# Kernel tuning notes

Measured on AMD Instinct MI355X. Metric: run time of the kernel, lower is better.

Reference implementation:

```python
import jax, jax.numpy as jnp
import numpy as np

N_QUBITS = 12
N_LAYERS = 3
HID = 16
IN_DIM = 6
BATCH = 4096
C64 = jnp.complex64


def _ry(t):
    c = jnp.cos(t / 2).astype(C64)
    s = jnp.sin(t / 2).astype(C64)
    return jnp.stack([jnp.stack([c, -s], -1), jnp.stack([s, c], -1)], -2)


def _rx(t):
    c = jnp.cos(t / 2).astype(C64)
    s = jnp.sin(t / 2).astype(C64)
    js = 1j * s
    return jnp.stack([jnp.stack([c, -js], -1), jnp.stack([-js, c], -1)], -2)


def _rz(t):
    e = jnp.exp(-1j * t.astype(C64) / 2)
    z = jnp.zeros_like(e)
    return jnp.stack([jnp.stack([e, z], -1), jnp.stack([z, jnp.conj(e)], -1)], -2)


def _apply_1q(state, U, wire):
    # state: (B,) + (2,)*n ; U: (2,2) shared or (B,2,2) per-sample
    s = jnp.moveaxis(state, wire + 1, 1)
    if U.ndim == 2:
        s = jnp.einsum('ij,bj...->bi...', U, s)
    else:
        s = jnp.einsum('bij,bj...->bi...', U, s)
    return jnp.moveaxis(s, 1, wire + 1)


def _cnot(state, c, t):
    ax_c = c + 1
    s0 = jnp.take(state, 0, axis=ax_c)
    s1 = jnp.take(state, 1, axis=ax_c)
    t_ax = t + 1 if t < c else t  # target axis after removing control axis
    s1 = jnp.flip(s1, axis=t_ax)  # X on target when control=1
    return jnp.stack([s0, s1], axis=ax_c)


def _quantum(angles, qparams):
    # angles: (B, n_qubits) angle-encoding RY rotations; qparams: (L, n, 3)
    B = angles.shape[0]
    n = N_QUBITS
    state = jnp.zeros((B,) + (2,) * n, C64).at[(slice(None),) + (0,) * n].set(1.0)
    for i in range(n):
        state = _apply_1q(state, _ry(angles[:, i]), i)
    for l in range(N_LAYERS):
        for i in range(n):
            # RX then RY then RZ on wire i -> fused 2x2
            U = _rz(qparams[l, i, 2]) @ _ry(qparams[l, i, 1]) @ _rx(qparams[l, i, 0])
            state = _apply_1q(state, U, i)
        for i in range(n - 1):
            state = _cnot(state, i, i + 1)
        if n > 2:
            state = _cnot(state, n - 1, 0)
    p = state.real ** 2 + state.imag ** 2  # (B,) + (2,)*n
    evs = []
    for i in range(n):
        axes = tuple(a for a in range(1, n + 1) if a != i + 1)
        pi = p.sum(axes)  # (B, 2)
        evs.append(pi[:, 0] - pi[:, 1])
    return jnp.stack(evs, axis=1)  # (B, n) PauliZ expvals


def setup_inputs() -> dict:
    key = jax.random.key(0)
    ks = jax.random.split(key, 14)
    w = lambda k, shape: jax.random.normal(k, shape, jnp.float32) * 0.1
    return {
        'x': jax.random.normal(ks[0], (BATCH, IN_DIM), jnp.float32),
        'W1': w(ks[1], (HID, IN_DIM)), 'b1': w(ks[2], (HID,)),
        'W2': w(ks[3], (HID, HID)), 'b2': w(ks[4], (HID,)),
        'W3': w(ks[5], (N_QUBITS, HID)), 'b3': w(ks[6], (N_QUBITS,)),
        'qparams': w(ks[7], (N_LAYERS, N_QUBITS, 3)),
        'P1': w(ks[8], (HID, N_QUBITS)), 'c1': w(ks[9], (HID,)),
        'P2': w(ks[10], (8, HID)), 'c2': w(ks[11], (8,)),
        'P3': w(ks[12], (1, 8)), 'c3': w(ks[13], (1,)),
    }


def reference(x, W1, b1, W2, b2, W3, b3, qparams, P1, c1, P2, c2, P3, c3):
    # classical preprocessor (dropout = identity at inference)
    h = jax.nn.relu(x @ W1.T + b1)
    h = jax.nn.relu(h @ W2.T + b2)
    angles = h @ W3.T + b3  # (B, n_qubits)
    q = _quantum(angles, qparams)  # (B, n_qubits)
    # classical postprocessor
    o = jax.nn.relu(q @ P1.T + c1)
    o = jax.nn.relu(o @ P2.T + c2)
    o = jax.nn.sigmoid(o @ P3.T + c3)
    return o.squeeze(-1)  # (B,)
```

## Files before the change

### kernel.cpp

```cpp
#include <hip/hip_runtime.h>
#include <stdint.h>

#define NQ   12
#define DIM  4096
#define TPB  256

typedef float   v2f   __attribute__((ext_vector_type(2)));
typedef float   v4f   __attribute__((ext_vector_type(4)));
typedef float   f32x4 __attribute__((ext_vector_type(4)));
typedef _Float16 v2h  __attribute__((ext_vector_type(2)));
typedef _Float16 f16x8 __attribute__((ext_vector_type(8)));
typedef uint32_t u32x4 __attribute__((ext_vector_type(4)));

struct PassP {
  uint16_t v[4];
  uint16_t m[4];
  uint16_t td[4];
  uint8_t  np[8];
  uint8_t  wire[4];
  uint8_t  layer;
  uint8_t  pad[3];
};
struct KP {
  PassP    pass[6];
  uint16_t ro_mask[12];
  uint8_t  ro_bin[12];
};

constexpr int chbit(uint32_t x) { int b = -1; for (int i = 0; i < 32; ++i) if ((x >> i) & 1u) b = i; return b; }

constexpr void bmm(uint32_t* C, const uint32_t* A, const uint32_t* B) {
  for (int i = 0; i < NQ; ++i) {
    uint32_t r = 0;
    for (int j = 0; j < NQ; ++j) if ((A[i] >> j) & 1u) r ^= B[j];
    C[i] = r;
  }
}
constexpr void binv(const uint32_t* M, uint32_t* Inv) {
  uint32_t A[NQ] = {}, I[NQ] = {};
  for (int i = 0; i < NQ; ++i) { A[i] = M[i]; I[i] = 1u << i; }
  for (int c = 0; c < NQ; ++c) {
    int piv = -1;
    for (int r = c; r < NQ; ++r) if ((A[r] >> c) & 1u) { piv = r; break; }
    if (piv < 0) continue;
    uint32_t ta = A[c]; A[c] = A[piv]; A[piv] = ta;
    uint32_t ti = I[c]; I[c] = I[piv]; I[piv] = ti;
    for (int r = 0; r < NQ; ++r)
      if (r != c && ((A[r] >> c) & 1u)) { A[r] ^= A[c]; I[r] ^= I[c]; }
  }
  for (int i = 0; i < NQ; ++i) Inv[i] = I[i];
}

constexpr int rank5(const uint32_t* cols, int n) {
  uint32_t rows[5] = {}; int rnk = 0;
  for (int q = 0; q < n; ++q) {
    uint32_t x = cols[q] & 31u;
    for (int bit = 4; bit >= 0; --bit) {
      if (!((x >> bit) & 1u)) continue;
      if (rows[bit]) { x ^= rows[bit]; }
      else { rows[bit] = x; ++rnk; break; }
    }
  }
  return rnk;
}

constexpr KP make_kp() {
  KP kp{};
  uint32_t A[NQ] = {}; A[0] = 0xFFEu;
  for (int i = 1; i < NQ; ++i) A[i] = (1u << (i + 1)) - 1u;
  uint32_t A2[NQ] = {}, A3[NQ] = {}, Ai[NQ] = {}, A2i[NQ] = {};
  bmm(A2, A, A); bmm(A3, A2, A);
  binv(A, Ai); binv(A2, A2i);

  uint32_t v5_0 = 0, v5_3 = 0, td5_1 = 0, td5_2 = 0;

  for (int p = 0; p < 6; ++p) {
    const int L = (p < 3) ? 1 : 2;
    const int wb = (p % 3) * 4;
    const uint32_t* M  = (L == 1) ? A  : A2;
    const uint32_t* Mi = (L == 1) ? Ai : A2i;
    uint32_t v0[4] = {}, m0[4] = {};
    for (int i = 0; i < 4; ++i) {
      int w = wb + i; uint32_t col = 0;
      for (int r = 0; r < NQ; ++r) col |= ((Mi[r] >> w) & 1u) << r;
      v0[i] = col; m0[i] = M[w];
    }
    uint32_t Bc[NQ] = {};
    for (int b = 0; b < NQ; ++b) {
      uint32_t col = 1u << b;
      for (int i = 0; i < 4; ++i) if ((m0[i] >> b) & 1u) col ^= v0[i];
      Bc[b] = col;
    }
    uint32_t redv[4] = {}; int pbit[4] = {}; uint32_t pivmask = 0;
    for (int i = 0; i < 4; ++i) {
      redv[i] = v0[i];
      for (int k2 = 0; k2 < i; ++k2) if ((redv[i] >> pbit[k2]) & 1u) redv[i] ^= redv[k2];
      pbit[i] = chbit(redv[i]); pivmask |= 1u << pbit[i];
    }
    uint8_t np0[8] = {}; int nc = 0;
    for (int b = 0; b < NQ; ++b) if (!((pivmask >> b) & 1u)) np0[nc++] = (uint8_t)b;

    int bestScore = -1;
    int bsel[4] = {0,1,2,3}; int bT0 = 4, bT1 = 5; int bperm[4] = {0,1,2,3};
    int cand = 0;
    for (int a = 0; a < 8; ++a) for (int b = a + 1; b < 8; ++b)
    for (int c = b + 1; c < 8; ++c) for (int d = c + 1; d < 8; ++d) {
      uint32_t jc[4] = {Bc[np0[a]], Bc[np0[b]], Bc[np0[c]], Bc[np0[d]]};
      int rJ = rank5(jc, 4);
      if (rJ < 4 && bestScore >= 0) continue;
      if (rJ == 4) { if (cand >= 4) continue; ++cand; }
      int rem[4] = {}; int rc2 = 0;
      for (int q = 0; q < 8; ++q) if (q != a && q != b && q != c && q != d) rem[rc2++] = q;
      const int tmax = (p == 5) ? 4 : 1;
      for (int t0 = 0; t0 < tmax; ++t0) for (int t1 = 0; t1 < tmax; ++t1) {
        if (p != 5) { if (t0 != 0 || t1 != 0) continue; }
        else if (t1 == t0) continue;
        const int rt0 = (p == 5) ? t0 : 0, rt1 = (p == 5) ? t1 : 1;
        for (int pa = 0; pa < 4; ++pa) for (int pb2 = 0; pb2 < 4; ++pb2) {
          if (pb2 == pa) continue;
          for (int pc = 0; pc < 4; ++pc) {
            if (pc == pa || pc == pb2) continue;
            const int pd = 6 - pa - pb2 - pc;
            uint32_t rd[6] = {jc[0], jc[1], jc[2], jc[3], v0[pc], v0[pd]};
            int rR = rank5(rd, 6);
            uint32_t wr[6] = {jc[0], jc[1], jc[2], jc[3], v0[pb2], v0[pc]};
            int rW = rank5(wr, 6);
            int rRO = 0;
            if (p == 5) {
              uint32_t roc[6] = {jc[0], jc[1], jc[2], jc[3], Bc[np0[rem[rt0]]], Bc[np0[rem[rt1]]]};
              rRO = rank5(roc, 6);
            }
            int score = rJ * 1000 + (rR == 5 ? 100 : 0) + (rW == 5 ? 10 : 0)
                      + (p == 5 ? (rRO == 5 ? 1 : 0) : 0);
            if (score > bestScore) {
              bestScore = score;
              bsel[0] = a; bsel[1] = b; bsel[2] = c; bsel[3] = d;
              bT0 = rem[rt0]; bT1 = rem[rt1];
              bperm[0] = pa; bperm[1] = pb2; bperm[2] = pc; bperm[3] = pd;
            }
          }
        }
      }
    }
    uint8_t npn[8] = {};
    npn[0] = np0[bsel[0]]; npn[1] = np0[bsel[1]];
    npn[2] = np0[bsel[2]]; npn[3] = np0[bsel[3]];
    npn[4] = np0[bT0]; npn[5] = np0[bT1];
    int cn = 6;
    for (int q = 0; q < 8; ++q) {
      bool used = (q == bsel[0] || q == bsel[1] || q == bsel[2] || q == bsel[3] ||
                   q == bT0 || q == bT1);
      if (!used) npn[cn++] = np0[q];
    }
    for (int q = 0; q < 8; ++q) kp.pass[p].np[q] = npn[q];
    for (int i = 0; i < 4; ++i) {
      kp.pass[p].v[i] = (uint16_t)v0[bperm[i]];
      kp.pass[p].m[i] = (uint16_t)m0[bperm[i]];
      kp.pass[p].wire[i] = (uint8_t)(wb + bperm[i]);
    }
    kp.pass[p].td[0] = 0;
    kp.pass[p].td[1] = (uint16_t)Bc[npn[4]];
    kp.pass[p].td[2] = (uint16_t)Bc[npn[5]];
    kp.pass[p].td[3] = (uint16_t)(Bc[npn[4]] ^ Bc[npn[5]]);
    kp.pass[p].layer = (uint8_t)L;
    if (p == 5) {
      v5_0 = v0[bperm[0]]; v5_3 = v0[bperm[3]];
      td5_1 = Bc[npn[4]]; td5_2 = Bc[npn[5]];
    }
  }
  for (int i = 0; i < NQ; ++i) kp.ro_mask[i] = (uint16_t)A3[i];
  for (int i = 0; i < NQ; ++i) {
    uint32_t b = 0;
    b |= (uint32_t)(__builtin_popcount(A3[i] & v5_0) & 1) << 0;
    b |= (uint32_t)(__builtin_popcount(A3[i] & v5_3) & 1) << 1;
    b |= (uint32_t)(__builtin_popcount(A3[i] & td5_1) & 1) << 2;
    b |= (uint32_t)(__builtin_popcount(A3[i] & td5_2) & 1) << 3;
    kp.ro_bin[i] = (uint8_t)b;
  }
  return kp;
}

constexpr KP kpc = make_kp();

__device__ __forceinline__ v2f cmulf(v2f a, v2f b) {
  return (v2f){a.x * b.x - a.y * b.y, a.x * b.y + a.y * b.x};
}
__device__ __forceinline__ uint32_t f2h2(float a, float b) {
  return __builtin_bit_cast(uint32_t, __builtin_amdgcn_cvt_pkrtz(a, b));
}
__device__ __forceinline__ uint32_t pk_rtn(float a, float b) {
  v2h h = {(_Float16)a, (_Float16)b};
  return __builtin_bit_cast(uint32_t, h);
}

__device__ __forceinline__ void build_u(const float* __restrict__ qp, int l, int w, float U[8]) {
  float p0 = qp[(l * 12 + w) * 3 + 0];
  float p1 = qp[(l * 12 + w) * 3 + 1];
  float p2 = qp[(l * 12 + w) * 3 + 2];
  float cx, sx, cy, sy, cz, sz;
  sincosf(0.5f * p0, &sx, &cx);
  sincosf(0.5f * p1, &sy, &cy);
  sincosf(0.5f * p2, &sz, &cz);
  float M00x =  cy * cx, M00y =  sy * sx;
  float M01x = -sy * cx, M01y = -cy * sx;
  float M10x =  sy * cx, M10y = -cy * sx;
  float M11x =  cy * cx, M11y = -sy * sx;
  U[0] = cz * M00x + sz * M00y; U[1] = cz * M00y - sz * M00x;
  U[2] = cz * M01x + sz * M01y; U[3] = cz * M01y - sz * M01x;
  U[4] = cz * M10x - sz * M10y; U[5] = cz * M10y + sz * M10x;
  U[6] = cz * M11x - sz * M11y; U[7] = cz * M11y + sz * M11x;
}

__device__ __forceinline__ int am_col(int c, int i) {
  return ((((c >> 2) ^ ((i >> 1) & 3)) << 2) | (c & 3));
}

template<int P, bool LAST>
__device__ __forceinline__ void do_pass(uint32_t* st, f16x8 a0, f16x8 a1,
                                        int lane, int wv, float* ev) {
  constexpr PassP pp = kpc.pass[P];
  const int t6 = (lane & 15) | (wv << 6);
  int rep = 0;
  #pragma unroll
  for (int k = 0; k < 8; ++k) rep |= ((t6 >> k) & 1) << pp.np[k];
  int base = rep;
  #pragma unroll
  for (int i = 0; i < 4; ++i)
    if (__popc(pp.m[i] & rep) & 1) base ^= pp.v[i];
  const int g = lane >> 4;
  const int cgr = ((g & 1) ? pp.v[2] : 0) ^ ((g & 2) ? pp.v[3] : 0);
  const int cgw = ((g & 1) ? pp.v[1] : 0) ^ ((g & 2) ? pp.v[2] : 0);
  float pr[16];
  const f32x4 z = {0.f, 0.f, 0.f, 0.f};
  #pragma unroll
  for (int T = 0; T < 4; ++T) {
    const int bT = base ^ pp.td[T];
    const int ra = bT ^ cgr;
    u32x4 braw = { st[ra], st[ra ^ pp.v[0]], st[ra ^ pp.v[1]],
                   st[ra ^ (pp.v[0] ^ pp.v[1])] };
    f16x8 bf = __builtin_bit_cast(f16x8, braw);
    f32x4 c0 = __builtin_amdgcn_mfma_f32_16x16x32_f16(a0, bf, z, 0, 0, 0);
    f32x4 c1 = __builtin_amdgcn_mfma_f32_16x16x32_f16(a1, bf, z, 0, 0, 0);
    if constexpr (!LAST) {
      const int wa = bT ^ cgw;
      st[wa]                      = f2h2(c0.x, c0.y);
      st[wa ^ pp.v[0]]            = f2h2(c0.z, c0.w);
      st[wa ^ pp.v[3]]            = f2h2(c1.x, c1.y);
      st[wa ^ (pp.v[3] ^ pp.v[0])] = f2h2(c1.z, c1.w);
    } else {
      const int nb = ((T & 1) << 2) | ((T >> 1) << 3);
      pr[nb]     = c0.x * c0.x + c0.y * c0.y;
      pr[nb | 1] = c0.z * c0.z + c0.w * c0.w;
      pr[nb | 2] = c1.x * c1.x + c1.y * c1.y;
      pr[nb | 3] = c1.z * c1.z + c1.w * c1.w;
    }
  }
  if constexpr (LAST) {
    #pragma unroll
    for (int gs = 1; gs < 16; gs <<= 1) {
      #pragma unroll
      for (int j = 0; j < 16; ++j) {
        if (j & gs) continue;
        float u = pr[j], w2 = pr[j | gs];
        pr[j] = u + w2; pr[j | gs] = u - w2;
      }
    }
    const int baseL = base ^ cgw;
    #pragma unroll
    for (int i = 0; i < NQ; ++i) {
      float h = pr[kpc.ro_bin[i]];
      int s = (__popc(kpc.ro_mask[i] & baseL) & 1) << 31;
      ev[i] = __int_as_float(__float_as_int(h) ^ s);
    }
  }
}

__global__ __launch_bounds__(TPB, 5) void hqc_kernel(
    const float* __restrict__ x,  const float* __restrict__ W1, const float* __restrict__ b1,
    const float* __restrict__ W2, const float* __restrict__ b2,
    const float* __restrict__ W3, const float* __restrict__ b3,
    const float* __restrict__ qp, const float* __restrict__ P1, const float* __restrict__ c1,
    const float* __restrict__ P2, const float* __restrict__ c2,
    const float* __restrict__ P3, const float* __restrict__ c3,
    float* __restrict__ out)
{
  __shared__ uint32_t st[DIM];
  __shared__ __align__(16) uint32_t Am[6][32][16];
  __shared__ v2f  gg[2][12][4];
  __shared__ v4f  gpk0[12][2];
  __shared__ float red[4][NQ];

  const int s    = blockIdx.x;
  const int t    = threadIdx.x;
  const int lane = t & 63;
  const int wv   = t >> 6;
  const int g    = lane >> 4;

  if (wv == 0) {
    if (lane < 16) {
      float a = b1[lane];
      #pragma unroll
      for (int k = 0; k < 6; ++k) a = fmaf(W1[lane * 6 + k], x[s * 6 + k], a);
      float h1 = fmaxf(a, 0.f);
      float a2 = b2[lane];
      #pragma unroll
      for (int k = 0; k < 16; ++k) a2 = fmaf(W2[lane * 16 + k], __shfl(h1, k, 64), a2);
      float h2 = fmaxf(a2, 0.f);
      const int lw = (lane < NQ) ? lane : 0;
      float a3 = b3[lw];
      #pragma unroll
      for (int k = 0; k < 16; ++k) a3 = fmaf(W3[lw * 16 + k], __shfl(h2, k, 64), a3);
      if (lane < NQ) {
        float U[8]; build_u(qp, 0, lane, U);
        float ca, sa; sincosf(0.5f * a3, &sa, &ca);
        float c0x = U[0] * ca + U[2] * sa, c0y = U[1] * ca + U[3] * sa;
        float c1x = U[4] * ca + U[6] * sa, c1y = U[5] * ca + U[7] * sa;
        gpk0[lane][0] = (v4f){c0x, c0x, -c0y, c0y};
        gpk0[lane][1] = (v4f){c1x, c1x, -c1y, c1y};
      }
    }
  } else if (wv <= 2) {
    if (lane < NQ) {
      float U[8]; build_u(qp, wv, lane, U);
      gg[wv - 1][lane][0] = (v2f){U[0], U[1]};
      gg[wv - 1][lane][1] = (v2f){U[2], U[3]};
      gg[wv - 1][lane][2] = (v2f){U[4], U[5]};
      gg[wv - 1][lane][3] = (v2f){U[6], U[7]};
    }
  }
  __syncthreads();

  {
    const int r_ = t >> 4, c_ = t & 15;
    #pragma unroll
    for (int p = 0; p < 6; ++p) {
      v2f e = (v2f){1.f, 0.f};
      #pragma unroll
      for (int i = 0; i < 4; ++i) {
        v2f u = gg[kpc.pass[p].layer - 1][kpc.pass[p].wire[i]]
                  [(((r_ >> i) & 1) << 1) | ((c_ >> i) & 1)];
        e = cmulf(e, u);
      }
      const int i0 = 2 * r_, i1 = 2 * r_ + 1;
      Am[p][i0][am_col(c_, i0)] = pk_rtn(e.x, -e.y);
      Am[p][i1][am_col(c_, i1)] = pk_rtn(e.y, e.x);
    }
  }

  {
    v2f acc = (v2f){1.f, 0.f};
    #pragma unroll
    for (int i = 0; i < 8; ++i) {
      v4f gk = gpk0[i][(t >> i) & 1];
      acc = gk.xy * acc + gk.zw * acc.yx;
    }
    v2f l16[16];
    l16[0] = acc;
    #pragma unroll
    for (int i = 0; i < 4; ++i) {
      v4f g0 = gpk0[8 + i][0], g1 = gpk0[8 + i][1];
      #pragma unroll
      for (int j = 0; j < (1 << i); ++j) {
        v2f a = l16[j];
        l16[j | (1 << i)] = g1.xy * a + g1.zw * a.yx;
        l16[j]            = g0.xy * a + g0.zw * a.yx;
      }
    }
    #pragma unroll
    for (int j = 0; j < 16; ++j) st[t | (j << 8)] = f2h2(l16[j].x, l16[j].y);
  }
  __syncthreads();

  f16x8 af[6][2];
  #pragma unroll
  for (int p = 0; p < 6; ++p) {
    #pragma unroll
    for (int Rb = 0; Rb < 2; ++Rb) {
      const int i = Rb * 16 + (lane & 15);
      const int q = g ^ ((i >> 1) & 3);
      const u32x4* src = reinterpret_cast<const u32x4*>(&Am[p][i][q * 4]);
      af[p][Rb] = __builtin_bit_cast(f16x8, *src);
    }
  }

  float ev[NQ];
  do_pass<0, false>(st, af[0][0], af[0][1], lane, wv, ev); __syncthreads();
  do_pass<1, false>(st, af[1][0], af[1][1], lane, wv, ev); __syncthreads();
  do_pass<2, false>(st, af[2][0], af[2][1], lane, wv, ev); __syncthreads();
  do_pass<3, false>(st, af[3][0], af[3][1], lane, wv, ev); __syncthreads();
  do_pass<4, false>(st, af[4][0], af[4][1], lane, wv, ev); __syncthreads();
  do_pass<5, true >(st, af[5][0], af[5][1], lane, wv, ev);

  #pragma unroll
  for (int off = 32; off >= 1; off >>= 1) {
    #pragma unroll
    for (int i = 0; i < NQ; ++i) ev[i] += __shfl_xor(ev[i], off, 64);
  }
  if (lane == 0) {
    #pragma unroll
    for (int i = 0; i < NQ; ++i) red[wv][i] = ev[i];
  }
  __syncthreads();

  if (wv == 0 && lane < 16) {
    float q = (lane < NQ)
      ? (red[0][lane] + red[1][lane] + red[2][lane] + red[3][lane])
      : 0.f;
    float a = c1[lane];
    #pragma unroll
    for (int j = 0; j < NQ; ++j) a = fmaf(P1[lane * NQ + j], __shfl(q, j, 64), a);
    float o1 = fmaxf(a, 0.f);
    float a2 = c2[lane & 7];
    #pragma unroll
    for (int j = 0; j < 16; ++j) a2 = fmaf(P2[(lane & 7) * 16 + j], __shfl(o1, j, 64), a2);
    float o2 = fmaxf(a2, 0.f);
    float a3 = c3[0];
    #pragma unroll
    for (int j = 0; j < 8; ++j) a3 = fmaf(P3[j], __shfl(o2, j, 64), a3);
    if (lane == 0) out[s] = 1.f / (1.f + expf(-a3));
  }
}

extern "C" void kernel_launch(void* const* d_in, const int* in_sizes, int n_in,
                              void* d_out, int out_size, void* d_ws, size_t ws_size,
                              hipStream_t stream) {
  (void)in_sizes; (void)n_in; (void)d_ws; (void)ws_size;
  hqc_kernel<<<out_size, TPB, 0, stream>>>(
      (const float*)d_in[0],  (const float*)d_in[1],  (const float*)d_in[2],
      (const float*)d_in[3],  (const float*)d_in[4],  (const float*)d_in[5],
      (const float*)d_in[6],  (const float*)d_in[7],  (const float*)d_in[8],
      (const float*)d_in[9],  (const float*)d_in[10], (const float*)d_in[11],
      (const float*)d_in[12], (const float*)d_in[13],
      (float*)d_out);
}
```

Before: 57.67 us.

## Double-buffer per-pass gate matrices and build them just in time

Instead of building all six 4-wire gate matrices up front and keeping them in registers, the kernel now keeps a two-slot LDS buffer and builds the next pass's matrix inside the current pass. The fragments are loaded from LDS at the start of each pass. This shrinks LDS and register use so launch bounds can rise from 5 to 7 blocks per CU. The compile-time basis search is also replaced by a penalty-based cost that no longer picks readout target columns, which may change the bank-conflict pattern of pass memory accesses.

```diff
diff --git a/kernel.cpp b/kernel.cpp
--- a/kernel.cpp
+++ b/kernel.cpp
@@ -21,10 +21,9 @@
   uint8_t  layer;
   uint8_t  pad[3];
 };
-struct KP {
-  PassP    pass[6];
-  uint16_t ro_mask[12];
-  uint8_t  ro_bin[12];
+struct ROC {
+  uint16_t mask[12];
+  uint8_t  bin[12];
 };
 
 constexpr int chbit(uint32_t x) { int b = -1; for (int i = 0; i < 32; ++i) if ((x >> i) & 1u) b = i; return b; }
@@ -63,124 +62,126 @@
   }
   return rnk;
 }
-
-constexpr KP make_kp() {
-  KP kp{};
+constexpr int penalty(int r) {
+  return r >= 5 ? 0 : r == 4 ? 58 : r == 3 ? 194 : r == 2 ? 469 : 1100;
+}
+
+constexpr PassP make_pass(int p) {
+  PassP pp{};
   uint32_t A[NQ] = {}; A[0] = 0xFFEu;
   for (int i = 1; i < NQ; ++i) A[i] = (1u << (i + 1)) - 1u;
-  uint32_t A2[NQ] = {}, A3[NQ] = {}, Ai[NQ] = {}, A2i[NQ] = {};
-  bmm(A2, A, A); bmm(A3, A2, A);
+  uint32_t A2[NQ] = {}, Ai[NQ] = {}, A2i[NQ] = {};
+  bmm(A2, A, A);
   binv(A, Ai); binv(A2, A2i);
 
-  uint32_t v5_0 = 0, v5_3 = 0, td5_1 = 0, td5_2 = 0;
-
-  for (int p = 0; p < 6; ++p) {
-    const int L = (p < 3) ? 1 : 2;
-    const int wb = (p % 3) * 4;
-    const uint32_t* M  = (L == 1) ? A  : A2;
-    const uint32_t* Mi = (L == 1) ? Ai : A2i;
-    uint32_t v0[4] = {}, m0[4] = {};
-    for (int i = 0; i < 4; ++i) {
-      int w = wb + i; uint32_t col = 0;
-      for (int r = 0; r < NQ; ++r) col |= ((Mi[r] >> w) & 1u) << r;
-      v0[i] = col; m0[i] = M[w];
-    }
-    uint32_t Bc[NQ] = {};
-    for (int b = 0; b < NQ; ++b) {
-      uint32_t col = 1u << b;
-      for (int i = 0; i < 4; ++i) if ((m0[i] >> b) & 1u) col ^= v0[i];
-      Bc[b] = col;
-    }
-    uint32_t redv[4] = {}; int pbit[4] = {}; uint32_t pivmask = 0;
-    for (int i = 0; i < 4; ++i) {
-      redv[i] = v0[i];
-      for (int k2 = 0; k2 < i; ++k2) if ((redv[i] >> pbit[k2]) & 1u) redv[i] ^= redv[k2];
-      pbit[i] = chbit(redv[i]); pivmask |= 1u << pbit[i];
-    }
-    uint8_t np0[8] = {}; int nc = 0;
-    for (int b = 0; b < NQ; ++b) if (!((pivmask >> b) & 1u)) np0[nc++] = (uint8_t)b;
-
-    int bestScore = -1;
-    int bsel[4] = {0,1,2,3}; int bT0 = 4, bT1 = 5; int bperm[4] = {0,1,2,3};
-    int cand = 0;
-    for (int a = 0; a < 8; ++a) for (int b = a + 1; b < 8; ++b)
-    for (int c = b + 1; c < 8; ++c) for (int d = c + 1; d < 8; ++d) {
-      uint32_t jc[4] = {Bc[np0[a]], Bc[np0[b]], Bc[np0[c]], Bc[np0[d]]};
-      int rJ = rank5(jc, 4);
-      if (rJ < 4 && bestScore >= 0) continue;
-      if (rJ == 4) { if (cand >= 4) continue; ++cand; }
-      int rem[4] = {}; int rc2 = 0;
-      for (int q = 0; q < 8; ++q) if (q != a && q != b && q != c && q != d) rem[rc2++] = q;
-      const int tmax = (p == 5) ? 4 : 1;
-      for (int t0 = 0; t0 < tmax; ++t0) for (int t1 = 0; t1 < tmax; ++t1) {
-        if (p != 5) { if (t0 != 0 || t1 != 0) continue; }
-        else if (t1 == t0) continue;
-        const int rt0 = (p == 5) ? t0 : 0, rt1 = (p == 5) ? t1 : 1;
-        for (int pa = 0; pa < 4; ++pa) for (int pb2 = 0; pb2 < 4; ++pb2) {
-          if (pb2 == pa) continue;
-          for (int pc = 0; pc < 4; ++pc) {
-            if (pc == pa || pc == pb2) continue;
-            const int pd = 6 - pa - pb2 - pc;
-            uint32_t rd[6] = {jc[0], jc[1], jc[2], jc[3], v0[pc], v0[pd]};
-            int rR = rank5(rd, 6);
-            uint32_t wr[6] = {jc[0], jc[1], jc[2], jc[3], v0[pb2], v0[pc]};
-            int rW = rank5(wr, 6);
-            int rRO = 0;
-            if (p == 5) {
-              uint32_t roc[6] = {jc[0], jc[1], jc[2], jc[3], Bc[np0[rem[rt0]]], Bc[np0[rem[rt1]]]};
-              rRO = rank5(roc, 6);
-            }
-            int score = rJ * 1000 + (rR == 5 ? 100 : 0) + (rW == 5 ? 10 : 0)
-                      + (p == 5 ? (rRO == 5 ? 1 : 0) : 0);
-            if (score > bestScore) {
-              bestScore = score;
-              bsel[0] = a; bsel[1] = b; bsel[2] = c; bsel[3] = d;
-              bT0 = rem[rt0]; bT1 = rem[rt1];
-              bperm[0] = pa; bperm[1] = pb2; bperm[2] = pc; bperm[3] = pd;
-            }
-          }
+  const int L = (p < 3) ? 1 : 2;
+  const int wb = (p % 3) * 4;
+  const uint32_t* M  = (L == 1) ? A  : A2;
+  const uint32_t* Mi = (L == 1) ? Ai : A2i;
+  uint32_t v0[4] = {}, m0[4] = {};
+  for (int i = 0; i < 4; ++i) {
+    int w = wb + i; uint32_t col = 0;
+    for (int r = 0; r < NQ; ++r) col |= ((Mi[r] >> w) & 1u) << r;
+    v0[i] = col; m0[i] = M[w];
+  }
+  uint32_t Bc[NQ] = {};
+  for (int b = 0; b < NQ; ++b) {
+    uint32_t col = 1u << b;
+    for (int i = 0; i < 4; ++i) if ((m0[i] >> b) & 1u) col ^= v0[i];
+    Bc[b] = col;
+  }
+  uint32_t redv[4] = {}; int pbit[4] = {}; uint32_t pivmask = 0;
+  for (int i = 0; i < 4; ++i) {
+    redv[i] = v0[i];
+    for (int k2 = 0; k2 < i; ++k2) if ((redv[i] >> pbit[k2]) & 1u) redv[i] ^= redv[k2];
+    pbit[i] = chbit(redv[i]); pivmask |= 1u << pbit[i];
+  }
+  uint8_t np0[8] = {}; int nc = 0;
+  for (int b = 0; b < NQ; ++b) if (!((pivmask >> b) & 1u)) np0[nc++] = (uint8_t)b;
+
+  int bestCost = 1 << 30;
+  int bsel[4] = {0, 1, 2, 3}; int bperm[4] = {0, 1, 2, 3};
+  for (int a = 0; a < 8; ++a) for (int b = a + 1; b < 8; ++b)
+  for (int c = b + 1; c < 8; ++c) for (int d = c + 1; d < 8; ++d) {
+    uint32_t jc[4] = {Bc[np0[a]], Bc[np0[b]], Bc[np0[c]], Bc[np0[d]]};
+    int prk[4][4] = {};
+    for (int i = 0; i < 4; ++i)
+      for (int j = i + 1; j < 4; ++j) {
+        uint32_t sp[6] = {jc[0], jc[1], jc[2], jc[3], v0[i], v0[j]};
+        prk[i][j] = prk[j][i] = rank5(sp, 6);
+      }
+    for (int pa = 0; pa < 4; ++pa) for (int pb2 = 0; pb2 < 4; ++pb2) {
+      if (pb2 == pa) continue;
+      for (int pc = 0; pc < 4; ++pc) {
+        if (pc == pa || pc == pb2) continue;
+        const int pd = 6 - pa - pb2 - pc;
+        const int cost = penalty(prk[pc][pd]) + penalty(prk[pb2][pc]);
+        if (cost < bestCost) {
+          bestCost = cost;
+          bsel[0] = a; bsel[1] = b; bsel[2] = c; bsel[3] = d;
+          bperm[0] = pa; bperm[1] = pb2; bperm[2] = pc; bperm[3] = pd;
         }
       }
     }
-    uint8_t npn[8] = {};
-    npn[0] = np0[bsel[0]]; npn[1] = np0[bsel[1]];
-    npn[2] = np0[bsel[2]]; npn[3] = np0[bsel[3]];
-    npn[4] = np0[bT0]; npn[5] = np0[bT1];
-    int cn = 6;
-    for (int q = 0; q < 8; ++q) {
-      bool used = (q == bsel[0] || q == bsel[1] || q == bsel[2] || q == bsel[3] ||
-                   q == bT0 || q == bT1);
-      if (!used) npn[cn++] = np0[q];
-    }
-    for (int q = 0; q < 8; ++q) kp.pass[p].np[q] = npn[q];
-    for (int i = 0; i < 4; ++i) {
-      kp.pass[p].v[i] = (uint16_t)v0[bperm[i]];
-      kp.pass[p].m[i] = (uint16_t)m0[bperm[i]];
-      kp.pass[p].wire[i] = (uint8_t)(wb + bperm[i]);
-    }
-    kp.pass[p].td[0] = 0;
-    kp.pass[p].td[1] = (uint16_t)Bc[npn[4]];
-    kp.pass[p].td[2] = (uint16_t)Bc[npn[5]];
-    kp.pass[p].td[3] = (uint16_t)(Bc[npn[4]] ^ Bc[npn[5]]);
-    kp.pass[p].layer = (uint8_t)L;
-    if (p == 5) {
-      v5_0 = v0[bperm[0]]; v5_3 = v0[bperm[3]];
-      td5_1 = Bc[npn[4]]; td5_2 = Bc[npn[5]];
-    }
-  }
-  for (int i = 0; i < NQ; ++i) kp.ro_mask[i] = (uint16_t)A3[i];
+  }
+  int rem[4] = {}; int rc2 = 0;
+  for (int q = 0; q < 8; ++q)
+    if (q != bsel[0] && q != bsel[1] && q != bsel[2] && q != bsel[3]) rem[rc2++] = q;
+
+  uint8_t npn[8] = {};
+  npn[0] = np0[bsel[0]]; npn[1] = np0[bsel[1]];
+  npn[2] = np0[bsel[2]]; npn[3] = np0[bsel[3]];
+  npn[4] = np0[rem[0]]; npn[5] = np0[rem[1]];
+  npn[6] = np0[rem[2]]; npn[7] = np0[rem[3]];
+  for (int q = 0; q < 8; ++q) pp.np[q] = npn[q];
+  for (int i = 0; i < 4; ++i) {
+    pp.v[i] = (uint16_t)v0[bperm[i]];
+    pp.m[i] = (uint16_t)m0[bperm[i]];
+    pp.wire[i] = (uint8_t)(wb + bperm[i]);
+  }
+  pp.td[0] = 0;
+  pp.td[1] = (uint16_t)Bc[npn[4]];
+  pp.td[2] = (uint16_t)Bc[npn[5]];
+  pp.td[3] = (uint16_t)(Bc[npn[4]] ^ Bc[npn[5]]);
+  pp.layer = (uint8_t)L;
+  return pp;
+}
+
+constexpr PassP kp0 = make_pass(0);
+constexpr PassP kp1 = make_pass(1);
+constexpr PassP kp2 = make_pass(2);
+constexpr PassP kp3 = make_pass(3);
+constexpr PassP kp4 = make_pass(4);
+constexpr PassP kp5 = make_pass(5);
+
+template<int P>
+constexpr PassP pget() {
+  if constexpr (P == 0) return kp0;
+  else if constexpr (P == 1) return kp1;
+  else if constexpr (P == 2) return kp2;
+  else if constexpr (P == 3) return kp3;
+  else if constexpr (P == 4) return kp4;
+  else return kp5;
+}
+
+constexpr ROC make_ro() {
+  ROC r{};
+  uint32_t A[NQ] = {}; A[0] = 0xFFEu;
+  for (int i = 1; i < NQ; ++i) A[i] = (1u << (i + 1)) - 1u;
+  uint32_t A2[NQ] = {}, A3[NQ] = {};
+  bmm(A2, A, A); bmm(A3, A2, A);
+  for (int i = 0; i < NQ; ++i) r.mask[i] = (uint16_t)A3[i];
   for (int i = 0; i < NQ; ++i) {
     uint32_t b = 0;
-    b |= (uint32_t)(__builtin_popcount(A3[i] & v5_0) & 1) << 0;
-    b |= (uint32_t)(__builtin_popcount(A3[i] & v5_3) & 1) << 1;
-    b |= (uint32_t)(__builtin_popcount(A3[i] & td5_1) & 1) << 2;
-    b |= (uint32_t)(__builtin_popcount(A3[i] & td5_2) & 1) << 3;
-    kp.ro_bin[i] = (uint8_t)b;
-  }
-  return kp;
-}
-
-constexpr KP kpc = make_kp();
+    b |= (uint32_t)(__builtin_popcount(A3[i] & (uint32_t)kp5.v[0]) & 1) << 0;
+    b |= (uint32_t)(__builtin_popcount(A3[i] & (uint32_t)kp5.v[3]) & 1) << 1;
+    b |= (uint32_t)(__builtin_popcount(A3[i] & (uint32_t)kp5.td[1]) & 1) << 2;
+    b |= (uint32_t)(__builtin_popcount(A3[i] & (uint32_t)kp5.td[2]) & 1) << 3;
+    r.bin[i] = (uint8_t)b;
+  }
+  return r;
+}
+constexpr ROC roc = make_ro();
 
 __device__ __forceinline__ v2f cmulf(v2f a, v2f b) {
   return (v2f){a.x * b.x - a.y * b.y, a.x * b.y + a.y * b.x};
@@ -215,10 +216,38 @@
   return ((((c >> 2) ^ ((i >> 1) & 3)) << 2) | (c & 3));
 }
 
+template<int P>
+__device__ __forceinline__ void build_am(uint32_t (*Am2)[32][16],
+                                         const v2f (*gg)[12][4], int t) {
+  constexpr PassP pp = pget<P>();
+  const int r_ = t >> 4, c_ = t & 15;
+  v2f e = (v2f){1.f, 0.f};
+  #pragma unroll
+  for (int i = 0; i < 4; ++i) {
+    v2f u = gg[pp.layer - 1][pp.wire[i]][(((r_ >> i) & 1) << 1) | ((c_ >> i) & 1)];
+    e = cmulf(e, u);
+  }
+  const int ra = 2 * r_, rb = 2 * r_ + 1;
+  Am2[P & 1][ra][am_col(c_, ra)] = pk_rtn(e.x, -e.y);
+  Am2[P & 1][rb][am_col(c_, rb)] = pk_rtn(e.y, e.x);
+}
+
 template<int P, bool LAST>
-__device__ __forceinline__ void do_pass(uint32_t* st, f16x8 a0, f16x8 a1,
-                                        int lane, int wv, float* ev) {
-  constexpr PassP pp = kpc.pass[P];
+__device__ __forceinline__ void do_pass(uint32_t* st, uint32_t (*Am2)[32][16],
+                                        const v2f (*gg)[12][4], int t, float* ev) {
+  constexpr PassP pp = pget<P>();
+  const int lane = t & 63;
+  const int wv   = t >> 6;
+  const int g    = lane >> 4;
+  f16x8 a0, a1;
+  {
+    const int li = lane & 15;
+    const int q0 = g ^ ((li >> 1) & 3);
+    a0 = __builtin_bit_cast(f16x8, *reinterpret_cast<const u32x4*>(&Am2[P & 1][li][q0 * 4]));
+    const int i1 = 16 + li;
+    const int q1 = g ^ ((i1 >> 1) & 3);
+    a1 = __builtin_bit_cast(f16x8, *reinterpret_cast<const u32x4*>(&Am2[P & 1][i1][q1 * 4]));
+  }
   const int t6 = (lane & 15) | (wv << 6);
   int rep = 0;
   #pragma unroll
@@ -227,7 +256,6 @@
   #pragma unroll
   for (int i = 0; i < 4; ++i)
     if (__popc(pp.m[i] & rep) & 1) base ^= pp.v[i];
-  const int g = lane >> 4;
   const int cgr = ((g & 1) ? pp.v[2] : 0) ^ ((g & 2) ? pp.v[3] : 0);
   const int cgw = ((g & 1) ? pp.v[1] : 0) ^ ((g & 2) ? pp.v[2] : 0);
   float pr[16];
@@ -243,9 +271,9 @@
     f32x4 c1 = __builtin_amdgcn_mfma_f32_16x16x32_f16(a1, bf, z, 0, 0, 0);
     if constexpr (!LAST) {
       const int wa = bT ^ cgw;
-      st[wa]                      = f2h2(c0.x, c0.y);
-      st[wa ^ pp.v[0]]            = f2h2(c0.z, c0.w);
-      st[wa ^ pp.v[3]]            = f2h2(c1.x, c1.y);
+      st[wa]                       = f2h2(c0.x, c0.y);
+      st[wa ^ pp.v[0]]             = f2h2(c0.z, c0.w);
+      st[wa ^ pp.v[3]]             = f2h2(c1.x, c1.y);
       st[wa ^ (pp.v[3] ^ pp.v[0])] = f2h2(c1.z, c1.w);
     } else {
       const int nb = ((T & 1) << 2) | ((T >> 1) << 3);
@@ -255,6 +283,7 @@
       pr[nb | 3] = c1.z * c1.z + c1.w * c1.w;
     }
   }
+  if constexpr (P < 5) build_am<P + 1>(Am2, gg, t);
   if constexpr (LAST) {
     #pragma unroll
     for (int gs = 1; gs < 16; gs <<= 1) {
@@ -268,14 +297,14 @@
     const int baseL = base ^ cgw;
     #pragma unroll
     for (int i = 0; i < NQ; ++i) {
-      float h = pr[kpc.ro_bin[i]];
-      int s = (__popc(kpc.ro_mask[i] & baseL) & 1) << 31;
+      float h = pr[roc.bin[i]];
+      int s = (__popc(roc.mask[i] & baseL) & 1) << 31;
       ev[i] = __int_as_float(__float_as_int(h) ^ s);
     }
   }
 }
 
-__global__ __launch_bounds__(TPB, 5) void hqc_kernel(
+__global__ __launch_bounds__(TPB, 7) void hqc_kernel(
     const float* __restrict__ x,  const float* __restrict__ W1, const float* __restrict__ b1,
     const float* __restrict__ W2, const float* __restrict__ b2,
     const float* __restrict__ W3, const float* __restrict__ b3,
@@ -285,7 +314,7 @@
     float* __restrict__ out)
 {
   __shared__ uint32_t st[DIM];
-  __shared__ __align__(16) uint32_t Am[6][32][16];
+  __shared__ __align__(16) uint32_t Am2[2][32][16];
   __shared__ v2f  gg[2][12][4];
   __shared__ v4f  gpk0[12][2];
   __shared__ float red[4][NQ];
@@ -294,7 +323,6 @@
   const int t    = threadIdx.x;
   const int lane = t & 63;
   const int wv   = t >> 6;
-  const int g    = lane >> 4;
 
   if (wv == 0) {
     if (lane < 16) {
@@ -330,23 +358,7 @@
   }
   __syncthreads();
 
-  {
-    const int r_ = t >> 4, c_ = t & 15;
-    #pragma unroll
-    for (int p = 0; p < 6; ++p) {
-      v2f e = (v2f){1.f, 0.f};
-      #pragma unroll
-      for (int i = 0; i < 4; ++i) {
-        v2f u = gg[kpc.pass[p].layer - 1][kpc.pass[p].wire[i]]
-                  [(((r_ >> i) & 1) << 1) | ((c_ >> i) & 1)];
-        e = cmulf(e, u);
-      }
-      const int i0 = 2 * r_, i1 = 2 * r_ + 1;
-      Am[p][i0][am_col(c_, i0)] = pk_rtn(e.x, -e.y);
-      Am[p][i1][am_col(c_, i1)] = pk_rtn(e.y, e.x);
-    }
-  }
-
+  build_am<0>(Am2, gg, t);
   {
     v2f acc = (v2f){1.f, 0.f};
     #pragma unroll
@@ -371,25 +383,13 @@
   }
   __syncthreads();
 
-  f16x8 af[6][2];
-  #pragma unroll
-  for (int p = 0; p < 6; ++p) {
-    #pragma unroll
-    for (int Rb = 0; Rb < 2; ++Rb) {
-      const int i = Rb * 16 + (lane & 15);
-      const int q = g ^ ((i >> 1) & 3);
-      const u32x4* src = reinterpret_cast<const u32x4*>(&Am[p][i][q * 4]);
-      af[p][Rb] = __builtin_bit_cast(f16x8, *src);
-    }
-  }
-
   float ev[NQ];
-  do_pass<0, false>(st, af[0][0], af[0][1], lane, wv, ev); __syncthreads();
-  do_pass<1, false>(st, af[1][0], af[1][1], lane, wv, ev); __syncthreads();
-  do_pass<2, false>(st, af[2][0], af[2][1], lane, wv, ev); __syncthreads();
-  do_pass<3, false>(st, af[3][0], af[3][1], lane, wv, ev); __syncthreads();
-  do_pass<4, false>(st, af[4][0], af[4][1], lane, wv, ev); __syncthreads();
-  do_pass<5, true >(st, af[5][0], af[5][1], lane, wv, ev);
+  do_pass<0, false>(st, Am2, gg, t, ev); __syncthreads();
+  do_pass<1, false>(st, Am2, gg, t, ev); __syncthreads();
+  do_pass<2, false>(st, Am2, gg, t, ev); __syncthreads();
+  do_pass<3, false>(st, Am2, gg, t, ev); __syncthreads();
+  do_pass<4, false>(st, Am2, gg, t, ev); __syncthreads();
+  do_pass<5, true >(st, Am2, gg, t, ev);
 
   #pragma unroll
   for (int off = 32; off >= 1; off >>= 1) {
```

New measurement: 54.36 us. 1.06x faster.
